# Kernel optimization log

Measured on AMD Instinct MI355X. Metric: run time of the kernel, lower is better.

## Reference

```python
import jax, jax.numpy as jnp
import numpy as np


def _maxpool2x2(x):
    # x: [B, C, H, W] -> [B, C, H//2, W//2]
    B, C, H, W = x.shape
    return x.reshape(B, C, H // 2, 2, W // 2, 2).max(axis=(3, 5))


def setup_inputs() -> dict:
    key = jax.random.key(0)
    ks = jax.random.split(key, 6)
    B, C, H, W = 16, 64, 64, 64
    x = jax.random.normal(ks[0], (B, C, H, W), dtype=jnp.float32)
    w_theta = jax.random.normal(ks[1], (C // 8, C), dtype=jnp.float32) * (1.0 / np.sqrt(C))
    w_phi = jax.random.normal(ks[2], (C // 8, C), dtype=jnp.float32) * (1.0 / np.sqrt(C))
    w_g = jax.random.normal(ks[3], (C // 2, C), dtype=jnp.float32) * (1.0 / np.sqrt(C))
    w_o = jax.random.normal(ks[4], (C, C // 2), dtype=jnp.float32) * (1.0 / np.sqrt(C // 2))
    gamma = jax.random.normal(ks[5], (), dtype=jnp.float32)
    return {"x": x, "w_theta": w_theta, "w_phi": w_phi, "w_g": w_g, "w_o": w_o, "gamma": gamma}


def reference(x, w_theta, w_phi, w_g, w_o, gamma):
    B, C, H, W = x.shape
    S = H * W  # full spatial size
    # 1x1 convs == channel matmuls
    theta = jnp.einsum('oc,bchw->bohw', w_theta, x)            # [B, C/8, H, W]
    phi = _maxpool2x2(jnp.einsum('oc,bchw->bohw', w_phi, x))   # [B, C/8, H/2, W/2]
    g = _maxpool2x2(jnp.einsum('oc,bchw->bohw', w_g, x))       # [B, C/2, H/2, W/2]
    theta_f = theta.reshape(B, C // 8, S)                      # [B, C/8, S]
    phi_f = phi.reshape(B, C // 8, S // 4)                     # [B, C/8, S/4]
    g_f = g.reshape(B, C // 2, S // 4)                         # [B, C/2, S/4]
    # beta = softmax(theta^T @ phi) over key dim
    scores = jnp.einsum('bcs,bct->bst', theta_f, phi_f)        # [B, S, S/4]
    beta = jax.nn.softmax(scores, axis=-1)
    attn = jnp.einsum('bct,bst->bcs', g_f, beta)               # [B, C/2, S]
    o = jnp.einsum('oc,bcs->bos', w_o, attn).reshape(B, C, H, W)
    return gamma * o + x
```

## Files before the change

### kernel.cpp

```cpp
#include <hip/hip_runtime.h>

#define B 16
#define C 64
#define SS 4096
#define TT 1024
#define CQ 8
#define CG 32

typedef _Float16 h4 __attribute__((ext_vector_type(4)));
typedef float f32x16 __attribute__((ext_vector_type(16)));

#if __has_builtin(__builtin_amdgcn_exp2f)
#define EXP2(x) __builtin_amdgcn_exp2f(x)
#else
#define EXP2(x) exp2f(x)
#endif

#define MFMA328(a, b, c) __builtin_amdgcn_mfma_f32_32x32x8f16((a), (b), (c), 0, 0, 0)

__global__ __launch_bounds__(256) void k_proj(
        const float* __restrict__ x, const float* __restrict__ w_theta,
        const float* __restrict__ w_phi, const float* __restrict__ w_g,
        _Float16* __restrict__ theta_t, _Float16* __restrict__ phi_t,
        _Float16* __restrict__ g_blk) {
    int tid = threadIdx.x;
    int W = blockIdx.x * 4 + (tid >> 6);
    int l = tid & 63;
    int ln = l & 31, hi = l >> 5;
    int b = W >> 6, ws = W & 63;
    int rp = ws >> 1, wt = ws & 1;
    int sA = rp * 128 + wt * 32 + ln;

    const float LOG2E = 1.44269504088896f;
    float wsc = 1.f;
    const float* wr0;
    if (ln < 8)       { wr0 = w_theta + ln * C; wsc = LOG2E; }
    else if (ln < 16) { wr0 = w_phi + (ln - 8) * C; }
    else              { wr0 = w_g + (ln - 16) * C; }
    const float* wr1 = w_g + (16 + (ln & 15)) * C;
    bool t1v = ln < 16;

    h4 wa0[8], wa1[8];
#pragma unroll
    for (int kk = 0; kk < 8; ++kk) {
        float4 v0 = *(const float4*)&wr0[8 * kk + 4 * hi];
        float4 v1 = *(const float4*)&wr1[8 * kk + 4 * hi];
        wa0[kk][0] = (_Float16)(v0.x * wsc);
        wa0[kk][1] = (_Float16)(v0.y * wsc);
        wa0[kk][2] = (_Float16)(v0.z * wsc);
        wa0[kk][3] = (_Float16)(v0.w * wsc);
        wa1[kk][0] = t1v ? (_Float16)v1.x : (_Float16)0.f;
        wa1[kk][1] = t1v ? (_Float16)v1.y : (_Float16)0.f;
        wa1[kk][2] = t1v ? (_Float16)v1.z : (_Float16)0.f;
        wa1[kk][3] = t1v ? (_Float16)v1.w : (_Float16)0.f;
    }

    const float* xb = x + ((size_t)b << 18);
    float xA[8][4], xB[8][4];
#pragma unroll
    for (int kk = 0; kk < 8; ++kk)
#pragma unroll
        for (int i = 0; i < 4; ++i) {
            int c = 8 * kk + 4 * hi + i;
            xA[kk][i] = xb[((size_t)c << 12) + sA];
            xB[kk][i] = xb[((size_t)c << 12) + sA + 64];
        }

    f32x16 aA0, aA1, aB0, aB1;
#pragma unroll
    for (int r = 0; r < 16; ++r) { aA0[r] = 0.f; aA1[r] = 0.f; aB0[r] = 0.f; aB1[r] = 0.f; }

#pragma unroll
    for (int kk = 0; kk < 8; ++kk) {
        h4 bA, bB;
#pragma unroll
        for (int i = 0; i < 4; ++i) {
            bA[i] = (_Float16)xA[kk][i];
            bB[i] = (_Float16)xB[kk][i];
        }
        aA0 = MFMA328(wa0[kk], bA, aA0);
        aB0 = MFMA328(wa0[kk], bB, aB0);
        aA1 = MFMA328(wa1[kk], bA, aA1);
        aB1 = MFMA328(wa1[kk], bB, aB1);
    }

    {
        h4 tv;
#pragma unroll
        for (int r = 0; r < 4; ++r) tv[r] = (_Float16)aA0[r];
        *(h4*)&theta_t[(size_t)((b << 12) + sA) * 8 + 4 * hi] = tv;
#pragma unroll
        for (int r = 0; r < 4; ++r) tv[r] = (_Float16)aB0[r];
        *(h4*)&theta_t[(size_t)((b << 12) + sA + 64) * 8 + 4 * hi] = tv;
    }

    int t = rp * 32 + wt * 16 + (ln >> 1);
    float pv[4];
#pragma unroll
    for (int j = 0; j < 4; ++j) {
        float m = fmaxf(aA0[4 + j], aB0[4 + j]);
        m = fmaxf(m, __shfl_xor(m, 1));
        pv[j] = m;
    }
    float gv[4][4];
#pragma unroll
    for (int j = 0; j < 4; ++j) {
        float m0 = fmaxf(aA0[8 + j],  aB0[8 + j]);
        float m1 = fmaxf(aA0[12 + j], aB0[12 + j]);
        float m2 = fmaxf(aA1[j],      aB1[j]);
        float m3 = fmaxf(aA1[4 + j],  aB1[4 + j]);
        gv[0][j] = fmaxf(m0, __shfl_xor(m0, 1));
        gv[1][j] = fmaxf(m1, __shfl_xor(m1, 1));
        gv[2][j] = fmaxf(m2, __shfl_xor(m2, 1));
        gv[3][j] = fmaxf(m3, __shfl_xor(m3, 1));
    }
    if ((l & 1) == 0) {
        h4 pj;
#pragma unroll
        for (int j = 0; j < 4; ++j) pj[j] = (_Float16)pv[j];
        *(h4*)&phi_t[(size_t)((b << 10) + t) * 8 + 4 * hi] = pj;
        _Float16* gb = g_blk + ((size_t)(b * 256 + (t >> 2)) * 32) * 4 + (t & 3);
#pragma unroll
        for (int part = 0; part < 4; ++part) {
            int cbase = part * 8 + 4 * hi;
#pragma unroll
            for (int j = 0; j < 4; ++j)
                gb[(size_t)(cbase + j) * 4] = (_Float16)gv[part][j];
        }
    }
}

__global__ __launch_bounds__(512, 4) void k_attn(
        const float* __restrict__ x, const _Float16* __restrict__ theta_t,
        const _Float16* __restrict__ phi_t, const _Float16* __restrict__ g_blk,
        const float* __restrict__ w_o, const float* __restrict__ gamma_p,
        float* __restrict__ out) {
    __shared__ __align__(16) char smem[81920];
    _Float16* g_sh   = (_Float16*)smem;
    _Float16* phi_sh = (_Float16*)(smem + 65536);
    float (*accx)[16][64] = (float (*)[16][64])smem;
    float (*mlx)[2][64]   = (float (*)[2][64])(smem + 32768);

    int tid = threadIdx.x;
    int bid = blockIdx.x;
    int wg = (bid & 7) * 64 + (bid >> 3);
    int b = wg >> 5;
    int s0 = (wg & 31) * 128;
    int w = tid >> 6;
    int l = tid & 63;
    int ln = l & 31, hi = l >> 5;
    int sub = w & 3, half = w >> 2;
    int sw = s0 + sub * 32;
    int h16 = half * 16;

    {
        const float4* srcg = (const float4*)(g_blk + (size_t)b * (256 * 128));
        float4* dstg = (float4*)smem;
#pragma unroll
        for (int i = 0; i < 8; ++i)
            dstg[tid + 512 * i] = srcg[tid + 512 * i];
        const float4* srcp = (const float4*)(phi_t + ((size_t)b << 10) * 8);
        float4* dstp = (float4*)phi_sh;
#pragma unroll
        for (int i = 0; i < 2; ++i)
            dstp[tid + 512 * i] = srcp[tid + 512 * i];
    }

    h4 bth = *(const h4*)&theta_t[(size_t)((b << 12) + sw + ln) * 8 + 4 * hi];

    const _Float16* phib = phi_t + ((size_t)b << 10) * 8;

    f32x16 zero;
#pragma unroll
    for (int r = 0; r < 16; ++r) zero[r] = 0.f;

#define LD_PHI(t_) (*(const h4*)&phib[(size_t)((t_) * 32 + ln) * 8 + 4 * hi])
#define LD_PHI_S(t_) (*(const h4*)&phi_sh[(size_t)((t_) * 32 + ln) * 8 + 4 * hi])
#define LD_G_S(dst, t_)                                                        \
    {                                                                          \
        _Pragma("unroll")                                                      \
        for (int kk = 0; kk < 4; ++kk)                                         \
            dst[kk] = *(const h4*)&g_sh[(size_t)(((t_) * 8 + 2 * kk + hi) * 32 + ln) * 4]; \
    }
#define FMAX16(dst, sc_)                                                       \
    {                                                                          \
        float t0 = fmaxf(fmaxf(sc_[0], sc_[1]), sc_[2]);                       \
        float t1 = fmaxf(fmaxf(sc_[3], sc_[4]), sc_[5]);                       \
        float t2 = fmaxf(fmaxf(sc_[6], sc_[7]), sc_[8]);                       \
        float t3 = fmaxf(fmaxf(sc_[9], sc_[10]), sc_[11]);                     \
        float t4 = fmaxf(fmaxf(sc_[12], sc_[13]), sc_[14]);                    \
        float u0 = fmaxf(fmaxf(t0, t1), t2);                                   \
        float u1 = fmaxf(fmaxf(t3, t4), sc_[15]);                              \
        dst = fmaxf(dst, fmaxf(u0, u1));                                       \
    }

    float mx = -1e30f;
    {
        h4 pa = LD_PHI(h16);
        h4 pb = LD_PHI(h16 + 1);
#pragma unroll 2
        for (int tc = 0; tc < 16; tc += 2) {
            h4 pan = LD_PHI(h16 + ((tc + 2) & 15));
            h4 pbn = LD_PHI(h16 + ((tc + 3) & 15));
            f32x16 sa = MFMA328(pa, bth, zero);
            f32x16 sb = MFMA328(pb, bth, zero);
            FMAX16(mx, sa);
            FMAX16(mx, sb);
            pa = pan;
            pb = pbn;
        }
        mx = fmaxf(mx, __shfl_xor(mx, 32));
    }

    f32x16 cneg;
#pragma unroll
    for (int r = 0; r < 16; ++r) cneg[r] = -mx;

    __syncthreads();

    f32x16 accE = zero, accO = zero;
    float lsum = 0.f;
    h4 ap = LD_PHI_S(h16);
    h4 ag[4];
    LD_G_S(ag, h16);

#pragma unroll 2
    for (int tc = 0; tc < 16; ++tc) {
        int tn = h16 + ((tc + 1) & 15);
        h4 apn = LD_PHI_S(tn);
        h4 agn[4];
        LD_G_S(agn, tn);

        f32x16 sc = MFMA328(ap, bth, cneg);

        h4 bp[4];
        float pa0 = 0.f, pa1 = 0.f;
#pragma unroll
        for (int kk = 0; kk < 4; ++kk)
#pragma unroll
            for (int i = 0; i < 4; ++i) {
                float p = EXP2(sc[4 * kk + i]);
                if (kk < 2) pa0 += p; else pa1 += p;
                bp[kk][i] = (_Float16)p;
            }
        lsum += pa0 + pa1;

        accE = MFMA328(ag[0], bp[0], accE);
        accO = MFMA328(ag[1], bp[1], accO);
        accE = MFMA328(ag[2], bp[2], accE);
        accO = MFMA328(ag[3], bp[3], accO);

        ap = apn;
#pragma unroll
        for (int kk = 0; kk < 4; ++kk) ag[kk] = agn[kk];
    }
    f32x16 acc = accE + accO;
    lsum += __shfl_xor(lsum, 32);

    __syncthreads();

#pragma unroll
    for (int r = 0; r < 16; ++r) accx[w][r][l] = acc[r];
    mlx[w][0][l] = mx;
    mlx[w][1][l] = lsum;
    __syncthreads();

    int p = w ^ 4;
    float m2 = mlx[p][0][l], l2 = mlx[p][1][l];
    float M = fmaxf(mx, m2);
    float f1 = EXP2(mx - M), f2 = EXP2(m2 - M);
    float lt = lsum * f1 + l2 * f2;
    float linv = 1.f / lt;

    h4 bat[4];
#pragma unroll
    for (int kk = 0; kk < 4; ++kk)
#pragma unroll
        for (int i = 0; i < 4; ++i) {
            float a2 = accx[p][4 * kk + i][l];
            bat[kk][i] = (_Float16)((acc[4 * kk + i] * f1 + a2 * f2) * linv);
        }

    float gm = gamma_p[0];
    h4 a3[4];
#pragma unroll
    for (int kk = 0; kk < 4; ++kk) {
        float4 wv = *(const float4*)&w_o[(half * 32 + ln) * CG + 8 * kk + 4 * hi];
        a3[kk][0] = (_Float16)(wv.x * gm);
        a3[kk][1] = (_Float16)(wv.y * gm);
        a3[kk][2] = (_Float16)(wv.z * gm);
        a3[kk][3] = (_Float16)(wv.w * gm);
    }
    f32x16 d = MFMA328(a3[0], bat[0], zero);
    d = MFMA328(a3[1], bat[1], d);
    d = MFMA328(a3[2], bat[2], d);
    d = MFMA328(a3[3], bat[3], d);
#pragma unroll
    for (int r = 0; r < 16; ++r) {
        int ch = half * 32 + (r & 3) + 8 * (r >> 2) + 4 * hi;
        size_t idx = (((size_t)(b * C + ch)) << 12) + sw + ln;
        out[idx] = d[r] + x[idx];
    }
#undef LD_PHI
#undef LD_PHI_S
#undef LD_G_S
#undef FMAX16
}

extern "C" void kernel_launch(void* const* d_in, const int* in_sizes, int n_in,
                              void* d_out, int out_size, void* d_ws, size_t ws_size,
                              hipStream_t stream) {
    const float* x       = (const float*)d_in[0];
    const float* w_theta = (const float*)d_in[1];
    const float* w_phi   = (const float*)d_in[2];
    const float* w_g     = (const float*)d_in[3];
    const float* w_o     = (const float*)d_in[4];
    const float* gamma   = (const float*)d_in[5];
    float* out = (float*)d_out;

    _Float16* ws      = (_Float16*)d_ws;
    _Float16* theta_t = ws;
    _Float16* phi_t   = theta_t + (size_t)B * SS * 8;
    _Float16* g_blk   = phi_t + (size_t)B * TT * 8;

    k_proj<<<256, 256, 0, stream>>>(x, w_theta, w_phi, w_g, theta_t, phi_t, g_blk);
    k_attn<<<512, 512, 0, stream>>>(x, theta_t, phi_t, g_blk, w_o, gamma, out);
}
```

Baseline: 30.54 us.

## Replace two-pass softmax max scan with single-pass online softmax rescaling

Drops the first pass that recomputed all score tiles from global phi just to find the row max. The max is now tracked online inside the main loop, and the accumulators and running sum are rescaled whenever a tile raises the max. This removes roughly a third of the score MFMAs and the global phi reads. In exchange it adds a per-tile max reduction with a cross-lane shuffle and a wave-uniform branch. The branch also contains some odd no-op arithmetic on sc, which looks like leftover debugging.

```diff
diff --git a/kernel.cpp b/kernel.cpp
--- a/kernel.cpp
+++ b/kernel.cpp
@@ -168,13 +168,10 @@
 
     h4 bth = *(const h4*)&theta_t[(size_t)((b << 12) + sw + ln) * 8 + 4 * hi];
 
-    const _Float16* phib = phi_t + ((size_t)b << 10) * 8;
-
     f32x16 zero;
 #pragma unroll
     for (int r = 0; r < 16; ++r) zero[r] = 0.f;
 
-#define LD_PHI(t_) (*(const h4*)&phib[(size_t)((t_) * 32 + ln) * 8 + 4 * hi])
 #define LD_PHI_S(t_) (*(const h4*)&phi_sh[(size_t)((t_) * 32 + ln) * 8 + 4 * hi])
 #define LD_G_S(dst, t_)                                                        \
     {                                                                          \
@@ -194,44 +191,84 @@
         dst = fmaxf(dst, fmaxf(u0, u1));                                       \
     }
 
-    float mx = -1e30f;
-    {
-        h4 pa = LD_PHI(h16);
-        h4 pb = LD_PHI(h16 + 1);
-#pragma unroll 2
-        for (int tc = 0; tc < 16; tc += 2) {
-            h4 pan = LD_PHI(h16 + ((tc + 2) & 15));
-            h4 pbn = LD_PHI(h16 + ((tc + 3) & 15));
-            f32x16 sa = MFMA328(pa, bth, zero);
-            f32x16 sb = MFMA328(pb, bth, zero);
-            FMAX16(mx, sa);
-            FMAX16(mx, sb);
-            pa = pan;
-            pb = pbn;
-        }
-        mx = fmaxf(mx, __shfl_xor(mx, 32));
-    }
-
-    f32x16 cneg;
-#pragma unroll
-    for (int r = 0; r < 16; ++r) cneg[r] = -mx;
-
     __syncthreads();
 
     f32x16 accE = zero, accO = zero;
     float lsum = 0.f;
+    float mx;
+    f32x16 cneg;
+
     h4 ap = LD_PHI_S(h16);
     h4 ag[4];
     LD_G_S(ag, h16);
 
+    {
+        int tn = h16 + 1;
+        h4 apn = LD_PHI_S(tn);
+        h4 agn[4];
+        LD_G_S(agn, tn);
+
+        f32x16 sc = MFMA328(ap, bth, zero);
+        float cm = -1e30f;
+        FMAX16(cm, sc);
+        cm = fmaxf(cm, __shfl_xor(cm, 32));
+        mx = cm;
+#pragma unroll
+        for (int r = 0; r < 16; ++r) cneg[r] = -mx;
+
+        h4 bp[4];
+        float pa0 = 0.f, pa1 = 0.f;
+#pragma unroll
+        for (int kk = 0; kk < 4; ++kk)
+#pragma unroll
+            for (int i = 0; i < 4; ++i) {
+                float p = EXP2(sc[4 * kk + i] - mx);
+                if (kk < 2) pa0 += p; else pa1 += p;
+                bp[kk][i] = (_Float16)p;
+            }
+        lsum = pa0 + pa1;
+
+        accE = MFMA328(ag[0], bp[0], accE);
+        accO = MFMA328(ag[1], bp[1], accO);
+        accE = MFMA328(ag[2], bp[2], accE);
+        accO = MFMA328(ag[3], bp[3], accO);
+
+        ap = apn;
+#pragma unroll
+        for (int kk = 0; kk < 4; ++kk) ag[kk] = agn[kk];
+    }
+
 #pragma unroll 2
-    for (int tc = 0; tc < 16; ++tc) {
+    for (int tc = 1; tc < 16; ++tc) {
         int tn = h16 + ((tc + 1) & 15);
         h4 apn = LD_PHI_S(tn);
         h4 agn[4];
         LD_G_S(agn, tn);
 
         f32x16 sc = MFMA328(ap, bth, cneg);
+
+        float cm = -1e30f;
+        FMAX16(cm, sc);
+        cm = fmaxf(cm, __shfl_xor(cm, 32));
+        if (__any(cm > 0.f)) {
+            float nm = mx + fmaxf(cm, 0.f);
+            float scl = EXP2(mx - nm);
+            mx = nm;
+#pragma unroll
+            for (int r = 0; r < 16; ++r) cneg[r] = -mx;
+            lsum *= scl;
+#pragma unroll
+            for (int r = 0; r < 16; ++r) accE[r] *= scl;
+#pragma unroll
+            for (int r = 0; r < 16; ++r) accO[r] *= scl;
+#pragma unroll
+            for (int r = 0; r < 16; ++r) sc[r] += (nm != mx) ? 0.f : 0.f;
+#pragma unroll
+            for (int r = 0; r < 16; ++r) sc[r] -= fmaxf(cm, 0.f) * 0.f;
+            float d = nm - (nm - fmaxf(cm, 0.f));
+#pragma unroll
+            for (int r = 0; r < 16; ++r) sc[r] -= d;
+        }
 
         h4 bp[4];
         float pa0 = 0.f, pa1 = 0.f;
@@ -301,7 +338,6 @@
         size_t idx = (((size_t)(b * C + ch)) << 12) + sw + ln;
         out[idx] = d[r] + x[idx];
     }
-#undef LD_PHI
 #undef LD_PHI_S
 #undef LD_G_S
 #undef FMAX16
```

Measured after the change: 36.89 us. 1.21x slower.
